# Kernel tuning notes

Hardware: AMD Instinct MI355X
Metric: run time of the kernel (lower is better)

Reference implementation:

```python
import jax, jax.numpy as jnp
import numpy as np

B, S, D, NH, NKV, HD = 1, 2048, 4096, 32, 8, 128
SCALE = HD ** -0.5


def setup_inputs() -> dict:
    key = jax.random.key(0)
    ks = jax.random.split(key, 5)
    sd = D ** -0.5
    x = jax.random.normal(ks[0], (B, S, D), jnp.float32)
    Wq = jax.random.normal(ks[1], (D, NH * HD), jnp.float32) * sd
    Wk = jax.random.normal(ks[2], (D, NKV * HD), jnp.float32) * sd
    Wv = jax.random.normal(ks[3], (D, NKV * HD), jnp.float32) * sd
    Wo = jax.random.normal(ks[4], (NH * HD, D), jnp.float32) * sd
    # real rotary tables (rotate-half convention), shape [S, HD]
    inv_freq = 1.0 / (10000.0 ** (np.arange(0, HD, 2, dtype=np.float64) / HD))
    ang = np.outer(np.arange(S, dtype=np.float64), inv_freq)  # [S, HD//2]
    emb = np.concatenate([ang, ang], axis=-1)  # [S, HD]
    cos = jnp.asarray(np.cos(emb), jnp.float32)
    sin = jnp.asarray(np.sin(emb), jnp.float32)
    return dict(x=x, Wq=Wq, Wk=Wk, Wv=Wv, Wo=Wo, cos=cos, sin=sin)


def _rope(t, cos, sin):
    # t: [B,S,H,HD]; cos/sin: [S,HD]
    c = cos[None, :, None, :]
    s = sin[None, :, None, :]
    t1, t2 = jnp.split(t, 2, axis=-1)
    rot = jnp.concatenate([-t2, t1], axis=-1)
    return t * c + rot * s


def _to_i8(t):
    # per-vector absmax quantization over last dim
    scale = 127.0 / jnp.clip(jnp.max(jnp.abs(t), axis=-1, keepdims=True), 1e-5, None)
    q = jnp.clip(jnp.round(t * scale), -128.0, 127.0).astype(jnp.int8)
    return q, scale


def reference(x, Wq, Wk, Wv, Wo, cos, sin):
    q = (x @ Wq).reshape(B, S, NH, HD)
    k = (x @ Wk).reshape(B, S, NKV, HD)
    v = (x @ Wv).reshape(B, S, NKV, HD)
    q = _rope(q, cos, sin)
    k = _rope(k, cos, sin)
    q_i8, q_s = _to_i8(q)          # [B,S,NH,HD], [B,S,NH,1]
    k_i8, k_s = _to_i8(k)          # [B,S,NKV,HD], [B,S,NKV,1]
    rep = NH // NKV                # GQA expansion
    k_i8 = jnp.repeat(k_i8, rep, axis=2)
    k_s = jnp.repeat(k_s, rep, axis=2)
    v = jnp.repeat(v, rep, axis=2)
    # int8 QK^T accumulated in int32 (exact), then per-vector dequant
    scores = jnp.einsum('bshd,bthd->bhst', q_i8, k_i8,
                        preferred_element_type=jnp.int32).astype(jnp.float32)
    q_st = jnp.transpose(q_s, (0, 2, 1, 3))            # [B,NH,S,1]
    k_st = jnp.transpose(k_s, (0, 2, 3, 1))            # [B,NH,1,S]
    scores = scores * (SCALE / (q_st * k_st))
    # causal mask (seq > 1, no cache so total == S)
    mask = jnp.triu(jnp.full((S, S), -jnp.inf, jnp.float32), k=1)
    scores = scores + mask
    attn = jax.nn.softmax(scores, axis=-1)             # [B,NH,S,S]
    out = jnp.einsum('bhst,bthd->bshd', attn, v).reshape(B, S, NH * HD)
    return out @ Wo
```

## Files before the change

### kernel.cpp

```cpp
#include <hip/hip_runtime.h>
#include <hip/hip_bf16.h>

#define S_LEN 2048
#define DMODEL 4096
#define NH 32
#define NKV 8
#define HD 128
#define NQKV 6144
#define ATT_SCALE_L2E 0.1275175213528852f

typedef __bf16 bf16x8 __attribute__((ext_vector_type(8)));
typedef __bf16 bf16x4 __attribute__((ext_vector_type(4)));
typedef float f32x4 __attribute__((ext_vector_type(4)));

__device__ __forceinline__ unsigned short f2b(float f) {
  union { float f; unsigned u; } a; a.f = f;
  unsigned u = a.u;
  return (unsigned short)((u + 0x7FFFu + ((u >> 16) & 1u)) >> 16);
}

__device__ __forceinline__ void gl16(const unsigned short* g, unsigned short* l) {
  __builtin_amdgcn_global_load_lds(
      (const __attribute__((address_space(1))) unsigned int*)g,
      (__attribute__((address_space(3))) unsigned int*)l, 16, 0, 0);
}

__global__ __launch_bounds__(256) void k_cvt_x(const float* __restrict__ x,
                                               unsigned short* __restrict__ xb) {
  int i = blockIdx.x * 256 + threadIdx.x;
  float4 v = ((const float4*)x)[i];
  ushort4 o;
  o.x = f2b(v.x); o.y = f2b(v.y); o.z = f2b(v.z); o.w = f2b(v.w);
  ((ushort4*)xb)[i] = o;
}

__global__ __launch_bounds__(256) void k_transpose(const float* __restrict__ W,
                                                   unsigned short* __restrict__ Wt,
                                                   int K, int N) {
  __shared__ float tile[64][65];
  int k0 = blockIdx.x * 64, n0 = blockIdx.y * 64;
  int tx = threadIdx.x & 31, ty = threadIdx.x >> 5;
#pragma unroll
  for (int i = 0; i < 8; ++i) {
    int k = ty + i * 8;
    const float* src = W + (size_t)(k0 + k) * N + n0;
    tile[k][tx] = src[tx];
    tile[k][tx + 32] = src[tx + 32];
  }
  __syncthreads();
  int kq = threadIdx.x & 15, nb = threadIdx.x >> 4;
#pragma unroll
  for (int i = 0; i < 4; ++i) {
    int n = nb + i * 16;
    ushort4 o;
    o.x = f2b(tile[kq * 4 + 0][n]);
    o.y = f2b(tile[kq * 4 + 1][n]);
    o.z = f2b(tile[kq * 4 + 2][n]);
    o.w = f2b(tile[kq * 4 + 3][n]);
    *(ushort4*)&Wt[(size_t)(n0 + n) * K + k0 + kq * 4] = o;
  }
}

__global__ __launch_bounds__(256) void k_vt(const unsigned short* __restrict__ v_bf,
                                            unsigned short* __restrict__ v_t) {
  __shared__ unsigned short tile[64][65];
  int s0 = blockIdx.x * 64, d0 = blockIdx.y * 64, kvh = blockIdx.z;
  int tx = threadIdx.x & 63, ty = threadIdx.x >> 6;
#pragma unroll
  for (int i = 0; i < 16; ++i) {
    int s = ty + i * 4;
    tile[s][tx] = v_bf[((size_t)(s0 + s) * NKV + kvh) * HD + d0 + tx];
  }
  __syncthreads();
#pragma unroll
  for (int i = 0; i < 16; ++i) {
    int d = ty + i * 4;
    v_t[((size_t)kvh * HD + d0 + d) * S_LEN + s0 + tx] = tile[tx][d];
  }
}

template <int FN>
__global__ __launch_bounds__(512, 2) void k_gemmN(const unsigned short* __restrict__ A,
                                                  const unsigned short* __restrict__ B,
                                                  float* __restrict__ C,
                                                  int M, int N, int K) {
  extern __shared__ __align__(16) unsigned short smem[];
  char* Sc = (char*)smem;
  const int tid = threadIdx.x;
  const int wvid = tid >> 6, l = tid & 63;
  const int wm = wvid >> 2, wn = wvid & 3;
  const int l15 = l & 15, l4 = l >> 4;

  const int nwg = gridDim.x;
  const int cpx = nwg >> 3;
  const int bid = blockIdx.x;
  const int swz = (bid & 7) * cpx + (bid >> 3);
  const int mtiles = M >> 8;
  const int m0 = (swz % mtiles) * 256;
  const int n0 = (swz / mtiles) * (FN * 64);

  const int NT = K >> 6;

  const int rsw = (l15 & 7) << 4;
  const int a_base = (wm * 64 + l15) * 128;
  const int b_base = (wn * FN * 16 + l15) * 128;
  const int c0 = (l4 * 16) ^ rsw;
  const int c1 = (64 + l4 * 16) ^ rsw;

  const int st_row = l >> 3;
  const int st_k8 = (l & 7) ^ st_row;

  auto stA = [&](int tt, int h) {
    if (tt >= NT) return;
    const unsigned short* g = A + (size_t)(m0 + h * 128) * K + tt * 64 + st_k8 * 8;
    unsigned short* lb = (unsigned short*)(Sc + (tt & 1) * 32768 + h * 16384);
#pragma unroll
    for (int j = 0; j < 2; ++j) {
      int blk = j * 8 + wvid;
      gl16(g + (size_t)(blk * 8 + st_row) * K, lb + blk * 512);
    }
  };
  auto stB = [&](int tt) {
    if (tt >= NT) return;
    const unsigned short* g = B + (size_t)n0 * K + tt * 64 + st_k8 * 8;
    unsigned short* lb = (unsigned short*)(Sc + 65536 + (tt & 1) * (FN * 8192));
#pragma unroll
    for (int j = 0; j < FN; ++j) {
      int blk = j * 8 + wvid;
      gl16(g + (size_t)(blk * 8 + st_row) * K, lb + blk * 512);
    }
  };

  f32x4 acc[2][4][FN] = {};

  stA(0, 0); stA(0, 1); stB(0);
  stA(1, 0); stA(1, 1);
  if (NT > 1) asm volatile("s_waitcnt vmcnt(4)" ::: "memory");
  else        asm volatile("s_waitcnt vmcnt(0)" ::: "memory");
  __builtin_amdgcn_s_barrier();

  for (int t = 0; t < NT; ++t) {
    const int b = t & 1;
    const char* Ab = Sc + b * 32768;
    const char* Bb = Sc + 65536 + b * (FN * 8192);
    bf16x8 a[4][2], bb[FN][2];

#pragma unroll
    for (int fm = 0; fm < 4; ++fm) {
      a[fm][0] = *(const bf16x8*)(Ab + a_base + fm * 2048 + c0);
      a[fm][1] = *(const bf16x8*)(Ab + a_base + fm * 2048 + c1);
    }
#pragma unroll
    for (int fn = 0; fn < FN; ++fn) {
      bb[fn][0] = *(const bf16x8*)(Bb + b_base + fn * 2048 + c0);
      bb[fn][1] = *(const bf16x8*)(Bb + b_base + fn * 2048 + c1);
    }
    stB(t + 1);
    __builtin_amdgcn_s_barrier();
    __builtin_amdgcn_s_setprio(1);
#pragma unroll
    for (int fm = 0; fm < 4; ++fm)
#pragma unroll
      for (int fn = 0; fn < FN; ++fn)
#pragma unroll
        for (int ks = 0; ks < 2; ++ks)
          acc[0][fm][fn] = __builtin_amdgcn_mfma_f32_16x16x32_bf16(a[fm][ks], bb[fn][ks], acc[0][fm][fn], 0, 0, 0);
    __builtin_amdgcn_s_setprio(0);
    __builtin_amdgcn_s_barrier();

#pragma unroll
    for (int fm = 0; fm < 4; ++fm) {
      a[fm][0] = *(const bf16x8*)(Ab + 16384 + a_base + fm * 2048 + c0);
      a[fm][1] = *(const bf16x8*)(Ab + 16384 + a_base + fm * 2048 + c1);
    }
    stA(t + 2, 0);
    __builtin_amdgcn_s_barrier();
    __builtin_amdgcn_s_setprio(1);
#pragma unroll
    for (int fm = 0; fm < 4; ++fm)
#pragma unroll
      for (int fn = 0; fn < FN; ++fn)
#pragma unroll
        for (int ks = 0; ks < 2; ++ks)
          acc[1][fm][fn] = __builtin_amdgcn_mfma_f32_16x16x32_bf16(a[fm][ks], bb[fn][ks], acc[1][fm][fn], 0, 0, 0);
    __builtin_amdgcn_s_setprio(0);
    __builtin_amdgcn_s_barrier();

    stA(t + 2, 1);
    if (t + 1 < NT) {
      if (t + 1 == NT - 1) asm volatile("s_waitcnt vmcnt(0)" ::: "memory");
      else                 asm volatile("s_waitcnt vmcnt(4)" ::: "memory");
      __builtin_amdgcn_s_barrier();
    }
  }

#pragma unroll
  for (int h = 0; h < 2; ++h)
#pragma unroll
    for (int fm = 0; fm < 4; ++fm) {
      int row0 = m0 + h * 128 + wm * 64 + fm * 16 + l4 * 4;
#pragma unroll
      for (int fn = 0; fn < FN; ++fn) {
        int col = n0 + wn * FN * 16 + fn * 16 + l15;
#pragma unroll
        for (int r = 0; r < 4; ++r)
          C[(size_t)(row0 + r) * N + col] = acc[h][fm][fn][r];
      }
    }
}

__global__ __launch_bounds__(256) void k_ropequant(const float* __restrict__ qkv,
                                                   const float* __restrict__ cost,
                                                   const float* __restrict__ sint,
                                                   unsigned short* __restrict__ q_int,
                                                   float* __restrict__ q_ds_t,
                                                   unsigned short* __restrict__ k_int,
                                                   float* __restrict__ k_ds_t,
                                                   unsigned short* __restrict__ v_bf) {
  int s = blockIdx.x;
  int wv = threadIdx.x >> 6, l = threadIdx.x & 63;
  int hh = blockIdx.y * 4 + wv;
  const float* row = qkv + (size_t)s * NQKV;
  if (hh < NH + NKV) {
    int off = (hh < NH) ? hh * HD : DMODEL + (hh - NH) * HD;
    float t1 = row[off + l], t2 = row[off + 64 + l];
    float c1 = cost[s * HD + l],      sn1 = sint[s * HD + l];
    float c2 = cost[s * HD + 64 + l], sn2 = sint[s * HD + 64 + l];
    float o1 = t1 * c1 - t2 * sn1;
    float o2 = t2 * c2 + t1 * sn2;
    float amax = fmaxf(fabsf(o1), fabsf(o2));
#pragma unroll
    for (int m = 1; m < 64; m <<= 1) amax = fmaxf(amax, __shfl_xor(amax, m));
    amax = fmaxf(amax, 1e-5f);
    float scale = 127.0f / amax;
    float dscale = amax * (1.0f / 127.0f);
    float v1 = fminf(fmaxf(rintf(o1 * scale), -128.f), 127.f);
    float v2 = fminf(fmaxf(rintf(o2 * scale), -128.f), 127.f);
    if (hh < NH) {
      unsigned short* dst = q_int + ((size_t)s * NH + hh) * HD;
      dst[l] = f2b(v1); dst[l + 64] = f2b(v2);
      if (l == 0) q_ds_t[(size_t)hh * S_LEN + s] = dscale;
    } else {
      int kh = hh - NH;
      unsigned short* dst = k_int + ((size_t)s * NKV + kh) * HD;
      dst[l] = f2b(v1); dst[l + 64] = f2b(v2);
      if (l == 0) k_ds_t[(size_t)kh * S_LEN + s] = dscale;
    }
  } else {
    int vh = hh - (NH + NKV);
    const float* src = row + DMODEL + NKV * HD + vh * HD;
    unsigned short* dst = v_bf + ((size_t)s * NKV + vh) * HD;
    dst[l] = f2b(src[l]);
    dst[l + 64] = f2b(src[l + 64]);
  }
}

__global__ __launch_bounds__(256) void k_attn(const unsigned short* __restrict__ q_int,
                                              const float* __restrict__ q_ds_t,
                                              const unsigned short* __restrict__ k_int,
                                              const float* __restrict__ k_ds_t,
                                              const unsigned short* __restrict__ v_t,
                                              unsigned short* __restrict__ o_bf) {
  __shared__ __align__(16) unsigned short K_lds[2][8192];
  __shared__ __align__(16) unsigned short V_lds[2][8192];
  __shared__ __align__(16) unsigned short P_lds[4][16 * 72];

  const int bid = blockIdx.x;
  const int kvh = bid & 7;
  const int ha = kvh * 4 + ((bid >> 3) & 1) * 2;
  const int qt = 31 - (bid >> 4);
  const int tid = threadIdx.x, wv = tid >> 6, l = tid & 63;
  const int l15 = l & 15, l4 = l >> 4;

  auto stage = [&](int b, int kt) {
    const unsigned short* kB = k_int + (size_t)kt * 64 * (NKV * HD) + kvh * HD;
    const unsigned short* vB = v_t + (size_t)kvh * HD * S_LEN + (size_t)kt * 64;
#pragma unroll
    for (int j = 0; j < 4; ++j) {
      int wi = j * 4 + wv;
      int slot = wi * 64 + l;
      int key = slot >> 4;
      int colb = ((slot & 15) * 16) ^ ((key & 7) << 4);
      gl16(kB + key * (NKV * HD) + (colb >> 1), &K_lds[b][wi * 512]);
      int d = slot >> 3;
      int ckb = ((slot & 7) * 16) ^ ((d & 7) << 4);
      gl16(vB + (size_t)d * S_LEN + (ckb >> 1), &V_lds[b][wi * 512]);
    }
  };

  const int qrow_lo = qt * 64 + wv * 16;
  const int qg = qrow_lo + l15;
  const int crow = qrow_lo + l4 * 4;

  bf16x8 qf[2][4];
  float qsS[2];
#pragma unroll
  for (int h2 = 0; h2 < 2; ++h2) {
    const unsigned short* qp = q_int + ((size_t)(qrow_lo + l15) * NH + ha + h2) * HD + l4 * 8;
#pragma unroll
    for (int kd = 0; kd < 4; ++kd) qf[h2][kd] = *(const bf16x8*)(qp + kd * 32);
    qsS[h2] = ATT_SCALE_L2E * q_ds_t[(size_t)(ha + h2) * S_LEN + qg];
  }

  float m_run[2] = {-3.0e38f, -3.0e38f};
  float l_run[2] = {0.f, 0.f};
  f32x4 o_acc[2][8] = {};

  const int nkt = qt + 1;
  stage(0, 0);
  __syncthreads();

  for (int kt = 0; kt < nkt; ++kt) {
    const int cur = kt & 1;
    f32x4 ksd[4];
    {
      const f32x4* kdp = (const f32x4*)(k_ds_t + (size_t)kvh * S_LEN + kt * 64 + l4 * 4);
#pragma unroll
      for (int nt = 0; nt < 4; ++nt) ksd[nt] = kdp[nt * 4];
    }
    if (kt + 1 < nkt) stage(cur ^ 1, kt + 1);

    f32x4 sacc[2][4] = {};
#pragma unroll
    for (int nt = 0; nt < 4; ++nt) {
      int key = nt * 16 + l15;
#pragma unroll
      for (int kd = 0; kd < 4; ++kd) {
        int byte = key * 256 + kd * 64 + l4 * 16;
        byte ^= (key & 7) << 4;
        bf16x8 kf = *(const bf16x8*)((const char*)&K_lds[cur][0] + byte);
        sacc[0][nt] = __builtin_amdgcn_mfma_f32_16x16x32_bf16(kf, qf[0][kd], sacc[0][nt], 0, 0, 0);
        sacc[1][nt] = __builtin_amdgcn_mfma_f32_16x16x32_bf16(kf, qf[1][kd], sacc[1][nt], 0, 0, 0);
      }
    }

    bf16x8 pa[2][2];
#pragma unroll
    for (int h2 = 0; h2 < 2; ++h2) {
      float p[4][4];
      float tmax = -3.0e38f;
#pragma unroll
      for (int nt = 0; nt < 4; ++nt) {
        int keyb = kt * 64 + nt * 16 + l4 * 4;
#pragma unroll
        for (int r = 0; r < 4; ++r) {
          float sc = sacc[h2][nt][r] * (qsS[h2] * ksd[nt][r]);
          sc = (keyb + r <= qg) ? sc : -3.0e38f;
          p[nt][r] = sc;
          tmax = fmaxf(tmax, sc);
        }
      }
      tmax = fmaxf(tmax, __shfl_xor(tmax, 16));
      tmax = fmaxf(tmax, __shfl_xor(tmax, 32));

      float nm = fmaxf(m_run[h2], tmax);
      bool need = tmax > m_run[h2] + 11.0f;
      if (__ballot(need)) {
        float corr = __builtin_amdgcn_exp2f(m_run[h2] - nm);
        m_run[h2] = nm;
        l_run[h2] *= corr;
        float cq[4];
#pragma unroll
        for (int r = 0; r < 4; ++r) cq[r] = __shfl(corr, (l & 48) | (l4 * 4 + r));
#pragma unroll
        for (int dt = 0; dt < 8; ++dt)
#pragma unroll
          for (int r = 0; r < 4; ++r) o_acc[h2][dt][r] *= cq[r];
      }

      float psum = 0.f;
#pragma unroll
      for (int nt = 0; nt < 4; ++nt)
#pragma unroll
        for (int r = 0; r < 4; ++r) {
          float e = __builtin_amdgcn_exp2f(p[nt][r] - m_run[h2]);
          p[nt][r] = e;
          psum += e;
        }
      psum += __shfl_xor(psum, 16);
      psum += __shfl_xor(psum, 32);
      l_run[h2] += psum;

#pragma unroll
      for (int nt = 0; nt < 4; ++nt) {
        bf16x4 pk;
        pk[0] = (__bf16)p[nt][0]; pk[1] = (__bf16)p[nt][1];
        pk[2] = (__bf16)p[nt][2]; pk[3] = (__bf16)p[nt][3];
        *(bf16x4*)((char*)&P_lds[wv][0] + l15 * 144 + nt * 32 + l4 * 8) = pk;
      }
#pragma unroll
      for (int kc = 0; kc < 2; ++kc)
        pa[h2][kc] = *(const bf16x8*)((const char*)&P_lds[wv][0] + l15 * 144 + kc * 64 + l4 * 16);
    }

#pragma unroll
    for (int dt = 0; dt < 8; ++dt) {
      int d = dt * 16 + l15;
      int swzv = (d & 7) << 4;
#pragma unroll
      for (int kc = 0; kc < 2; ++kc) {
        int byte = d * 128 + ((kc * 64 + l4 * 16) ^ swzv);
        bf16x8 vb = *(const bf16x8*)((const char*)&V_lds[cur][0] + byte);
        o_acc[0][dt] = __builtin_amdgcn_mfma_f32_16x16x32_bf16(pa[0][kc], vb, o_acc[0][dt], 0, 0, 0);
        o_acc[1][dt] = __builtin_amdgcn_mfma_f32_16x16x32_bf16(pa[1][kc], vb, o_acc[1][dt], 0, 0, 0);
      }
    }
    __syncthreads();
  }

#pragma unroll
  for (int h2 = 0; h2 < 2; ++h2) {
    float inv = 1.0f / l_run[h2];
    float invq[4];
#pragma unroll
    for (int r = 0; r < 4; ++r) invq[r] = __shfl(inv, (l & 48) | (l4 * 4 + r));
#pragma unroll
    for (int dt = 0; dt < 8; ++dt)
#pragma unroll
      for (int r = 0; r < 4; ++r)
        o_bf[(size_t)(crow + r) * (NH * HD) + (ha + h2) * HD + dt * 16 + l15] =
            f2b(o_acc[h2][dt][r] * invq[r]);
  }
}

extern "C" void kernel_launch(void* const* d_in, const int* in_sizes, int n_in,
                              void* d_out, int out_size, void* d_ws, size_t ws_size,
                              hipStream_t stream) {
  const float* x    = (const float*)d_in[0];
  const float* Wq   = (const float*)d_in[1];
  const float* Wk   = (const float*)d_in[2];
  const float* Wv   = (const float*)d_in[3];
  const float* Wo   = (const float*)d_in[4];
  const float* cost = (const float*)d_in[5];
  const float* sint = (const float*)d_in[6];
  float* out = (float*)d_out;
  char* ws = (char*)d_ws;

  unsigned short* xb     = (unsigned short*)(ws);
  unsigned short* wqkv_t = (unsigned short*)(ws + 16777216);
  unsigned short* wo_t   = (unsigned short*)(ws + 67108864);
  float*          qkv    = (float*)(ws + 100663296);
  unsigned short* q_int  = (unsigned short*)(ws + 150994944);
  unsigned short* k_int  = (unsigned short*)(ws + 167772160);
  unsigned short* v_bf   = (unsigned short*)(ws + 171966464);
  float*          q_ds_t = (float*)(ws + 176160768);
  float*          k_ds_t = (float*)(ws + 176422912);
  unsigned short* o_bf   = (unsigned short*)(ws + 176488448);
  unsigned short* v_t    = (unsigned short*)(ws);

  hipFuncSetAttribute((const void*)k_gemmN<3>,
                      hipFuncAttributeMaxDynamicSharedMemorySize, 114688);
  hipFuncSetAttribute((const void*)k_gemmN<2>,
                      hipFuncAttributeMaxDynamicSharedMemorySize, 98304);

  k_cvt_x<<<(S_LEN * DMODEL / 4) / 256, 256, 0, stream>>>(x, xb);
  k_transpose<<<dim3(64, 64), 256, 0, stream>>>(Wq, wqkv_t, 4096, 4096);
  k_transpose<<<dim3(64, 16), 256, 0, stream>>>(Wk, wqkv_t + (size_t)4096 * 4096, 4096, 1024);
  k_transpose<<<dim3(64, 16), 256, 0, stream>>>(Wv, wqkv_t + (size_t)5120 * 4096, 4096, 1024);
  k_transpose<<<dim3(64, 64), 256, 0, stream>>>(Wo, wo_t, 4096, 4096);
  k_gemmN<3><<<dim3(256), 512, 114688, stream>>>(xb, wqkv_t, qkv, 2048, 6144, 4096);
  k_ropequant<<<dim3(2048, 12), 256, 0, stream>>>(qkv, cost, sint, q_int, q_ds_t, k_int, k_ds_t, v_bf);
  k_vt<<<dim3(32, 2, 8), 256, 0, stream>>>(v_bf, v_t);
  k_attn<<<dim3(512), 256, 0, stream>>>(q_int, q_ds_t, k_int, k_ds_t, v_t, o_bf);
  k_gemmN<2><<<dim3(256), 512, 98304, stream>>>(o_bf, wo_t, out, 2048, 4096, 4096);
}
```

Measured before the change: 340.7 us.

## Use 128-row GEMM tile for QKV projection with bf16 output

Replaces the QKV projection GEMM with a new kernel that uses 128-row M tiles, 512 workgroups and launch bounds allowing more resident blocks. The kernel writes bf16 instead of fp32, and the rope/quant kernel now reads bf16 and copies V directly without conversion. This aims to improve occupancy and wave balance and to halve the intermediate QKV traffic. In exchange it adds rounding of Q/K before rope and quantization, which can shift int8 values, and the smaller tile reduces data reuse per block.

```diff
diff --git a/kernel.cpp b/kernel.cpp
--- a/kernel.cpp
+++ b/kernel.cpp
@@ -17,6 +17,9 @@
   union { float f; unsigned u; } a; a.f = f;
   unsigned u = a.u;
   return (unsigned short)((u + 0x7FFFu + ((u >> 16) & 1u)) >> 16);
+}
+__device__ __forceinline__ float b2f(unsigned short u) {
+  union { unsigned u; float f; } a; a.u = (unsigned)u << 16; return a.f;
 }
 
 __device__ __forceinline__ void gl16(const unsigned short* g, unsigned short* l) {
@@ -76,6 +79,112 @@
   for (int i = 0; i < 16; ++i) {
     int d = ty + i * 4;
     v_t[((size_t)kvh * HD + d0 + d) * S_LEN + s0 + tx] = tile[tx][d];
+  }
+}
+
+template <int FN, bool BF16OUT>
+__global__ __launch_bounds__(512, 4) void k_g128(const unsigned short* __restrict__ A,
+                                                 const unsigned short* __restrict__ B,
+                                                 void* __restrict__ Cv,
+                                                 int M, int N, int K) {
+  extern __shared__ __align__(16) unsigned short smem[];
+  char* Sc = (char*)smem;
+  const int tid = threadIdx.x;
+  const int wvid = tid >> 6, l = tid & 63;
+  const int wm = wvid >> 2, wn = wvid & 3;
+  const int l15 = l & 15, l4 = l >> 4;
+
+  const int cpx = gridDim.x >> 3;
+  const int swz = (blockIdx.x & 7) * cpx + (blockIdx.x >> 3);
+  const int mtiles = M >> 7;
+  const int m0 = (swz % mtiles) * 128;
+  const int n0 = (swz / mtiles) * (FN * 64);
+
+  const int NT = K >> 6;
+
+  const int rsw = (l15 & 7) << 4;
+  const int a_base = (wm * 64 + l15) * 128;
+  const int b_base = (wn * FN * 16 + l15) * 128;
+  const int c0 = (l4 * 16) ^ rsw;
+  const int c1 = (64 + l4 * 16) ^ rsw;
+
+  const int srow = l >> 3;
+  const int st_k8 = (l & 7) ^ (srow & 7);
+
+  auto stA = [&](int tt) {
+    if (tt >= NT) return;
+    const unsigned short* g = A + (size_t)(m0 + wvid * 8 + srow) * K + tt * 64 + st_k8 * 8;
+    char* lb = Sc + (tt & 1) * 16384 + wvid * 1024;
+#pragma unroll
+    for (int j = 0; j < 2; ++j)
+      gl16(g + (size_t)(j * 64) * K, (unsigned short*)(lb + j * 8192));
+  };
+  auto stB = [&](int tt) {
+    if (tt >= NT) return;
+    const unsigned short* g = B + (size_t)(n0 + wvid * 8 + srow) * K + tt * 64 + st_k8 * 8;
+    char* lb = Sc + 32768 + (tt & 1) * (FN * 8192) + wvid * 1024;
+#pragma unroll
+    for (int j = 0; j < FN; ++j)
+      gl16(g + (size_t)(j * 64) * K, (unsigned short*)(lb + j * 8192));
+  };
+
+  f32x4 acc[4][FN] = {};
+
+  stA(0); stB(0); stA(1);
+  if (NT > 1) asm volatile("s_waitcnt vmcnt(2)" ::: "memory");
+  else        asm volatile("s_waitcnt vmcnt(0)" ::: "memory");
+  __builtin_amdgcn_s_barrier();
+
+  for (int t = 0; t < NT; ++t) {
+    const char* Ab = Sc + (t & 1) * 16384;
+    const char* Bb = Sc + 32768 + (t & 1) * (FN * 8192);
+    stB(t + 1);
+    bf16x8 a[4], b[FN];
+#pragma unroll
+    for (int fm = 0; fm < 4; ++fm) a[fm] = *(const bf16x8*)(Ab + a_base + fm * 2048 + c0);
+#pragma unroll
+    for (int fn = 0; fn < FN; ++fn) b[fn] = *(const bf16x8*)(Bb + b_base + fn * 2048 + c0);
+    __builtin_amdgcn_s_setprio(1);
+#pragma unroll
+    for (int fm = 0; fm < 4; ++fm)
+#pragma unroll
+      for (int fn = 0; fn < FN; ++fn)
+        acc[fm][fn] = __builtin_amdgcn_mfma_f32_16x16x32_bf16(a[fm], b[fn], acc[fm][fn], 0, 0, 0);
+    __builtin_amdgcn_s_setprio(0);
+#pragma unroll
+    for (int fm = 0; fm < 4; ++fm) a[fm] = *(const bf16x8*)(Ab + a_base + fm * 2048 + c1);
+#pragma unroll
+    for (int fn = 0; fn < FN; ++fn) b[fn] = *(const bf16x8*)(Bb + b_base + fn * 2048 + c1);
+    __builtin_amdgcn_s_setprio(1);
+#pragma unroll
+    for (int fm = 0; fm < 4; ++fm)
+#pragma unroll
+      for (int fn = 0; fn < FN; ++fn)
+        acc[fm][fn] = __builtin_amdgcn_mfma_f32_16x16x32_bf16(a[fm], b[fn], acc[fm][fn], 0, 0, 0);
+    __builtin_amdgcn_s_setprio(0);
+    __builtin_amdgcn_s_barrier();
+    stA(t + 2);
+    if (t + 1 < NT) {
+      if (t + 1 == NT - 1) asm volatile("s_waitcnt vmcnt(0)" ::: "memory");
+      else                 asm volatile("s_waitcnt vmcnt(2)" ::: "memory");
+      __builtin_amdgcn_s_barrier();
+    }
+  }
+
+#pragma unroll
+  for (int fm = 0; fm < 4; ++fm) {
+    int row0 = m0 + wm * 64 + fm * 16 + l4 * 4;
+#pragma unroll
+    for (int fn = 0; fn < FN; ++fn) {
+      int col = n0 + wn * FN * 16 + fn * 16 + l15;
+#pragma unroll
+      for (int r = 0; r < 4; ++r) {
+        if constexpr (BF16OUT)
+          ((unsigned short*)Cv)[(size_t)(row0 + r) * N + col] = f2b(acc[fm][fn][r]);
+        else
+          ((float*)Cv)[(size_t)(row0 + r) * N + col] = acc[fm][fn][r];
+      }
+    }
   }
 }
 
@@ -209,7 +318,7 @@
     }
 }
 
-__global__ __launch_bounds__(256) void k_ropequant(const float* __restrict__ qkv,
+__global__ __launch_bounds__(256) void k_ropequant(const unsigned short* __restrict__ qkv,
                                                    const float* __restrict__ cost,
                                                    const float* __restrict__ sint,
                                                    unsigned short* __restrict__ q_int,
@@ -220,10 +329,10 @@
   int s = blockIdx.x;
   int wv = threadIdx.x >> 6, l = threadIdx.x & 63;
   int hh = blockIdx.y * 4 + wv;
-  const float* row = qkv + (size_t)s * NQKV;
+  const unsigned short* row = qkv + (size_t)s * NQKV;
   if (hh < NH + NKV) {
     int off = (hh < NH) ? hh * HD : DMODEL + (hh - NH) * HD;
-    float t1 = row[off + l], t2 = row[off + 64 + l];
+    float t1 = b2f(row[off + l]), t2 = b2f(row[off + 64 + l]);
     float c1 = cost[s * HD + l],      sn1 = sint[s * HD + l];
     float c2 = cost[s * HD + 64 + l], sn2 = sint[s * HD + 64 + l];
     float o1 = t1 * c1 - t2 * sn1;
@@ -248,10 +357,10 @@
     }
   } else {
     int vh = hh - (NH + NKV);
-    const float* src = row + DMODEL + NKV * HD + vh * HD;
+    const unsigned short* src = row + DMODEL + NKV * HD + vh * HD;
     unsigned short* dst = v_bf + ((size_t)s * NKV + vh) * HD;
-    dst[l] = f2b(src[l]);
-    dst[l + 64] = f2b(src[l + 64]);
+    dst[l] = src[l];
+    dst[l + 64] = src[l + 64];
   }
 }
 
@@ -439,7 +548,7 @@
   unsigned short* xb     = (unsigned short*)(ws);
   unsigned short* wqkv_t = (unsigned short*)(ws + 16777216);
   unsigned short* wo_t   = (unsigned short*)(ws + 67108864);
-  float*          qkv    = (float*)(ws + 100663296);
+  unsigned short* qkv    = (unsigned short*)(ws + 100663296);
   unsigned short* q_int  = (unsigned short*)(ws + 150994944);
   unsigned short* k_int  = (unsigned short*)(ws + 167772160);
   unsigned short* v_bf   = (unsigned short*)(ws + 171966464);
@@ -448,8 +557,8 @@
   unsigned short* o_bf   = (unsigned short*)(ws + 176488448);
   unsigned short* v_t    = (unsigned short*)(ws);
 
-  hipFuncSetAttribute((const void*)k_gemmN<3>,
-                      hipFuncAttributeMaxDynamicSharedMemorySize, 114688);
+  hipFuncSetAttribute((const void*)k_g128<3, true>,
+                      hipFuncAttributeMaxDynamicSharedMemorySize, 81920);
   hipFuncSetAttribute((const void*)k_gemmN<2>,
                       hipFuncAttributeMaxDynamicSharedMemorySize, 98304);
 
@@ -458,7 +567,7 @@
   k_transpose<<<dim3(64, 16), 256, 0, stream>>>(Wk, wqkv_t + (size_t)4096 * 4096, 4096, 1024);
   k_transpose<<<dim3(64, 16), 256, 0, stream>>>(Wv, wqkv_t + (size_t)5120 * 4096, 4096, 1024);
   k_transpose<<<dim3(64, 64), 256, 0, stream>>>(Wo, wo_t, 4096, 4096);
-  k_gemmN<3><<<dim3(256), 512, 114688, stream>>>(xb, wqkv_t, qkv, 2048, 6144, 4096);
+  k_g128<3, true><<<dim3(512), 512, 81920, stream>>>(xb, wqkv_t, qkv, 2048, 6144, 4096);
   k_ropequant<<<dim3(2048, 12), 256, 0, stream>>>(qkv, cost, sint, q_int, q_ds_t, k_int, k_ds_t, v_bf);
   k_vt<<<dim3(32, 2, 8), 256, 0, stream>>>(v_bf, v_t);
   k_attn<<<dim3(512), 256, 0, stream>>>(q_int, q_ds_t, k_int, k_ds_t, v_t, o_bf);
```

Result: no change. 338.7 us (-0.6%).
